# Kernel tuning notes

Hardware: AMD Instinct MI355X
Metric: run time of the kernel (lower is better)

The kernel has to match this reference:

```python
import jax, jax.numpy as jnp
import numpy as np

N_NODES = 50000
N_GRAPHS = 512


def gcn_conv(x, W, b, row, col, norm, n_nodes):
    # PyG GCNConv: h = x @ W; out_i = sum_{j->i} norm_ij * h_j + b
    h = x @ W  # [N, H]
    msgs = h[row] * norm[:, None]  # gather source features, scale
    out = jax.ops.segment_sum(msgs, col, num_segments=n_nodes)
    return out + b


def reference(x, edge_index, batch, W0, b0, W1, b1, W2, b2, Wf, bf):
    n = x.shape[0]
    src, dst = edge_index[0], edge_index[1]
    # add self loops
    loop = jnp.arange(n)
    row = jnp.concatenate([src, loop])
    col = jnp.concatenate([dst, loop])
    # symmetric degree normalization: 1/sqrt(deg_i * deg_j)
    deg = jax.ops.segment_sum(jnp.ones_like(col, dtype=x.dtype), col, num_segments=n)
    dis = jnp.where(deg > 0, 1.0 / jnp.sqrt(deg), 0.0)
    norm = dis[row] * dis[col]

    h = x
    for W, b in ((W0, b0), (W1, b1), (W2, b2)):
        h = jax.nn.relu(gcn_conv(h, W, b, row, col, norm, n))
        # dropout is identity in eval mode

    # global mean pool over graphs
    sums = jax.ops.segment_sum(h, batch, num_segments=N_GRAPHS)
    counts = jax.ops.segment_sum(jnp.ones((n,), dtype=h.dtype), batch, num_segments=N_GRAPHS)
    pooled = sums / jnp.maximum(counts, 1.0)[:, None]  # [B, H]

    logits = pooled @ Wf + bf
    return jax.nn.log_softmax(logits, axis=1)


def setup_inputs() -> dict:
    key = jax.random.key(0)
    ks = jax.random.split(key, 12)
    d_in, d_h, d_out = 128, 128, 10
    x = jax.random.normal(ks[0], (N_NODES, d_in), dtype=jnp.float32)
    edge_index = jax.random.randint(ks[1], (2, 600000), 0, N_NODES, dtype=jnp.int64)
    batch = jnp.sort(jax.random.randint(ks[2], (N_NODES,), 0, N_GRAPHS, dtype=jnp.int64))
    s = 1.0 / np.sqrt(d_h)
    return {
        "x": x,
        "edge_index": edge_index,
        "batch": batch,
        "W0": jax.random.normal(ks[3], (d_in, d_h), dtype=jnp.float32) * s,
        "b0": jnp.zeros((d_h,), dtype=jnp.float32),
        "W1": jax.random.normal(ks[4], (d_h, d_h), dtype=jnp.float32) * s,
        "b1": jnp.zeros((d_h,), dtype=jnp.float32),
        "W2": jax.random.normal(ks[5], (d_h, d_h), dtype=jnp.float32) * s,
        "b2": jnp.zeros((d_h,), dtype=jnp.float32),
        "Wf": jax.random.normal(ks[6], (d_h, d_out), dtype=jnp.float32) * s,
        "bf": jnp.zeros((d_out,), dtype=jnp.float32),
    }
```

## Files before the change

### kernel.cpp

```cpp
#include <hip/hip_runtime.h>
#include <hip/hip_bf16.h>

#define NN 50000
#define NE 600000
#define NG 512

typedef __attribute__((ext_vector_type(8))) short bf16x8;
typedef __attribute__((ext_vector_type(4))) float f32x4;

__device__ __forceinline__ float bf_lo(unsigned u) {
    unsigned v = u << 16;
    return __builtin_bit_cast(float, v);
}
__device__ __forceinline__ float bf_hi(unsigned u) {
    unsigned v = u & 0xFFFF0000u;
    return __builtin_bit_cast(float, v);
}
__device__ __forceinline__ unsigned f2bf(float f) {
    unsigned u = __builtin_bit_cast(unsigned, f);
    return (u + 0x7FFFu + ((u >> 16) & 1u)) >> 16;
}

__global__ __launch_bounds__(256) void k_zero(float* p, int n) {
    int i = blockIdx.x * 256 + threadIdx.x;
    if (i < n) p[i] = 0.0f;
}

__global__ __launch_bounds__(256) void k_histcnt(const int* __restrict__ dst, int* __restrict__ deg,
                                                 const int* __restrict__ batch, float* __restrict__ counts) {
    int i = blockIdx.x * 256 + threadIdx.x;
    if (i < NE) atomicAdd(&deg[dst[i]], 1);
    if (i < NN) atomicAdd(&counts[batch[i]], 1.0f);
}

__global__ __launch_bounds__(256) void k_alloc(const int* __restrict__ deg, int* __restrict__ gcur,
                                               int* __restrict__ rowstart, int* __restrict__ cursor,
                                               float* __restrict__ dis, uint2* __restrict__ cpk) {
    int i = blockIdx.x * 256 + threadIdx.x;
    if (i >= NN) return;
    int d = deg[i];
    int dr = (d + 7) & ~7;
    int st = atomicAdd(gcur, dr);
    rowstart[i] = st;
    cursor[i] = st;
    dis[i] = 1.0f / sqrtf((float)(d + 1));
    for (int p = st + d; p < st + dr; ++p) cpk[p] = make_uint2(0u, 0u);
}

__global__ __launch_bounds__(256) void k_fill(const int* __restrict__ src, const int* __restrict__ dst,
                                              const float* __restrict__ dis, int* __restrict__ cursor,
                                              uint2* __restrict__ cpk) {
    int e = blockIdx.x * 256 + threadIdx.x;
    if (e >= NE) return;
    int s = src[e], d = dst[e];
    int slot = atomicAdd(&cursor[d], 1);
    cpk[slot] = make_uint2((unsigned)s, __builtin_bit_cast(unsigned, dis[s] * dis[d]));
}

__global__ __launch_bounds__(256) void k_cvt_x(const float4* __restrict__ in, uint2* __restrict__ out, int n4) {
    int i = blockIdx.x * 256 + threadIdx.x;
    if (i >= n4) return;
    float4 v = in[i];
    uint2 o;
    o.x = f2bf(v.x) | (f2bf(v.y) << 16);
    o.y = f2bf(v.z) | (f2bf(v.w) << 16);
    out[i] = o;
}

__global__ __launch_bounds__(256) void k_cvt_w(const float* __restrict__ W0, const float* __restrict__ W1,
                                               const float* __restrict__ W2, unsigned short* __restrict__ Wt) {
    int idx = blockIdx.x * 256 + threadIdx.x;
    if (idx >= 3 * 16384) return;
    int m = idx >> 14;
    int r = idx & 16383;
    int k = r >> 7, c = r & 127;
    const float* W = (m == 0) ? W0 : (m == 1) ? W1 : W2;
    Wt[m * 16384 + c * 128 + k] = (unsigned short)f2bf(W[k * 128 + c]);
}

__global__ __launch_bounds__(256) void k_gemm_mfma(const unsigned short* __restrict__ A,
                                                   const unsigned short* __restrict__ Wt,
                                                   unsigned short* __restrict__ C, int M) {
    int wave = threadIdx.x >> 6;
    int lane = threadIdx.x & 63;
    int rowbase = blockIdx.x * 64 + wave * 16;
    int lr = lane & 15;
    int kg = lane >> 4;

    int arow = rowbase + lr;
    if (arow >= M) arow = M - 1;
    bf16x8 a[4];
#pragma unroll
    for (int kt = 0; kt < 4; ++kt)
        a[kt] = *(const bf16x8*)&A[arow * 128 + kt * 32 + kg * 8];

    f32x4 acc[8];
#pragma unroll
    for (int nt = 0; nt < 8; ++nt) acc[nt] = (f32x4){0.f, 0.f, 0.f, 0.f};

#pragma unroll
    for (int nt = 0; nt < 8; ++nt) {
        const unsigned short* wp = &Wt[(nt * 16 + lr) * 128 + kg * 8];
#pragma unroll
        for (int kt = 0; kt < 4; ++kt) {
            bf16x8 b = *(const bf16x8*)&wp[kt * 32];
            acc[nt] = __builtin_amdgcn_mfma_f32_16x16x32_bf16(a[kt], b, acc[nt], 0, 0, 0);
        }
    }

    int crow0 = rowbase + (lane >> 4) * 4;
#pragma unroll
    for (int nt = 0; nt < 8; ++nt) {
#pragma unroll
        for (int r = 0; r < 4; ++r) {
            int gr = crow0 + r;
            if (gr < M) C[gr * 128 + nt * 16 + lr] = (unsigned short)f2bf(acc[nt][r]);
        }
    }
}

template <int POOL>
__global__ __launch_bounds__(256) void k_gather(const uint2* __restrict__ h,
                                                const int* __restrict__ rowstart,
                                                const int* __restrict__ rowend,
                                                const uint2* __restrict__ cpk,
                                                const float* __restrict__ dis,
                                                const float* __restrict__ bias,
                                                uint2* __restrict__ outbuf,
                                                const int* __restrict__ batch,
                                                float* __restrict__ sums) {
    int t = blockIdx.x * 256 + threadIdx.x;
    int node = t >> 5;
    if (node >= NN) return;
    int f = t & 31;

    int s0 = rowstart[node];
    int e0 = rowend[node];

    float acc[8][4];
#pragma unroll
    for (int j = 0; j < 8; ++j)
#pragma unroll
        for (int k = 0; k < 4; ++k) acc[j][k] = 0.f;

    const uint4* mp = (const uint4*)cpk;
    uint4 m0, m1, m2, m3;
    {
        int b = s0 >> 1;
        m0 = mp[b]; m1 = mp[b + 1]; m2 = mp[b + 2]; m3 = mp[b + 3];
    }

    for (int s = s0; s < e0; s += 8) {
        uint4 c0 = m0, c1 = m1, c2 = m2, c3 = m3;
        int sn = s + 8;
        int b = (sn < e0 ? sn : s0) >> 1;
        m0 = mp[b]; m1 = mp[b + 1]; m2 = mp[b + 2]; m3 = mp[b + 3];

        uint2 v0 = h[(int)c0.x * 32 + f];
        uint2 v1 = h[(int)c0.z * 32 + f];
        uint2 v2 = h[(int)c1.x * 32 + f];
        uint2 v3 = h[(int)c1.z * 32 + f];
        uint2 v4 = h[(int)c2.x * 32 + f];
        uint2 v5 = h[(int)c2.z * 32 + f];
        uint2 v6 = h[(int)c3.x * 32 + f];
        uint2 v7 = h[(int)c3.z * 32 + f];
        float w0 = __builtin_bit_cast(float, c0.y);
        float w1 = __builtin_bit_cast(float, c0.w);
        float w2 = __builtin_bit_cast(float, c1.y);
        float w3 = __builtin_bit_cast(float, c1.w);
        float w4 = __builtin_bit_cast(float, c2.y);
        float w5 = __builtin_bit_cast(float, c2.w);
        float w6 = __builtin_bit_cast(float, c3.y);
        float w7 = __builtin_bit_cast(float, c3.w);

        acc[0][0] = fmaf(bf_lo(v0.x), w0, acc[0][0]);
        acc[0][1] = fmaf(bf_hi(v0.x), w0, acc[0][1]);
        acc[0][2] = fmaf(bf_lo(v0.y), w0, acc[0][2]);
        acc[0][3] = fmaf(bf_hi(v0.y), w0, acc[0][3]);
        acc[1][0] = fmaf(bf_lo(v1.x), w1, acc[1][0]);
        acc[1][1] = fmaf(bf_hi(v1.x), w1, acc[1][1]);
        acc[1][2] = fmaf(bf_lo(v1.y), w1, acc[1][2]);
        acc[1][3] = fmaf(bf_hi(v1.y), w1, acc[1][3]);
        acc[2][0] = fmaf(bf_lo(v2.x), w2, acc[2][0]);
        acc[2][1] = fmaf(bf_hi(v2.x), w2, acc[2][1]);
        acc[2][2] = fmaf(bf_lo(v2.y), w2, acc[2][2]);
        acc[2][3] = fmaf(bf_hi(v2.y), w2, acc[2][3]);
        acc[3][0] = fmaf(bf_lo(v3.x), w3, acc[3][0]);
        acc[3][1] = fmaf(bf_hi(v3.x), w3, acc[3][1]);
        acc[3][2] = fmaf(bf_lo(v3.y), w3, acc[3][2]);
        acc[3][3] = fmaf(bf_hi(v3.y), w3, acc[3][3]);
        acc[4][0] = fmaf(bf_lo(v4.x), w4, acc[4][0]);
        acc[4][1] = fmaf(bf_hi(v4.x), w4, acc[4][1]);
        acc[4][2] = fmaf(bf_lo(v4.y), w4, acc[4][2]);
        acc[4][3] = fmaf(bf_hi(v4.y), w4, acc[4][3]);
        acc[5][0] = fmaf(bf_lo(v5.x), w5, acc[5][0]);
        acc[5][1] = fmaf(bf_hi(v5.x), w5, acc[5][1]);
        acc[5][2] = fmaf(bf_lo(v5.y), w5, acc[5][2]);
        acc[5][3] = fmaf(bf_hi(v5.y), w5, acc[5][3]);
        acc[6][0] = fmaf(bf_lo(v6.x), w6, acc[6][0]);
        acc[6][1] = fmaf(bf_hi(v6.x), w6, acc[6][1]);
        acc[6][2] = fmaf(bf_lo(v6.y), w6, acc[6][2]);
        acc[6][3] = fmaf(bf_hi(v6.y), w6, acc[6][3]);
        acc[7][0] = fmaf(bf_lo(v7.x), w7, acc[7][0]);
        acc[7][1] = fmaf(bf_hi(v7.x), w7, acc[7][1]);
        acc[7][2] = fmaf(bf_lo(v7.y), w7, acc[7][2]);
        acc[7][3] = fmaf(bf_hi(v7.y), w7, acc[7][3]);
    }

    float d = dis[node];
    float ws = d * d;
    uint2 hv = h[node * 32 + f];
    acc[0][0] = fmaf(bf_lo(hv.x), ws, acc[0][0]);
    acc[0][1] = fmaf(bf_hi(hv.x), ws, acc[0][1]);
    acc[0][2] = fmaf(bf_lo(hv.y), ws, acc[0][2]);
    acc[0][3] = fmaf(bf_hi(hv.y), ws, acc[0][3]);

    float a0 = ((acc[0][0] + acc[1][0]) + (acc[2][0] + acc[3][0])) +
               ((acc[4][0] + acc[5][0]) + (acc[6][0] + acc[7][0]));
    float a1 = ((acc[0][1] + acc[1][1]) + (acc[2][1] + acc[3][1])) +
               ((acc[4][1] + acc[5][1]) + (acc[6][1] + acc[7][1]));
    float a2 = ((acc[0][2] + acc[1][2]) + (acc[2][2] + acc[3][2])) +
               ((acc[4][2] + acc[5][2]) + (acc[6][2] + acc[7][2]));
    float a3 = ((acc[0][3] + acc[1][3]) + (acc[2][3] + acc[3][3])) +
               ((acc[4][3] + acc[5][3]) + (acc[6][3] + acc[7][3]));

    float4 b = ((const float4*)bias)[f];
    a0 = fmaxf(a0 + b.x, 0.f);
    a1 = fmaxf(a1 + b.y, 0.f);
    a2 = fmaxf(a2 + b.z, 0.f);
    a3 = fmaxf(a3 + b.w, 0.f);

    if (POOL == 0) {
        uint2 o;
        o.x = f2bf(a0) | (f2bf(a1) << 16);
        o.y = f2bf(a2) | (f2bf(a3) << 16);
        outbuf[node * 32 + f] = o;
    } else {
        int g = batch[node];
        float* o = sums + g * 128 + f * 4;
        atomicAdd(o + 0, a0);
        atomicAdd(o + 1, a1);
        atomicAdd(o + 2, a2);
        atomicAdd(o + 3, a3);
    }
}

__global__ __launch_bounds__(64) void k_head(const float* __restrict__ sums,
                                             const float* __restrict__ counts,
                                             const float* __restrict__ Wf,
                                             const float* __restrict__ bf,
                                             float* __restrict__ out) {
    int g = blockIdx.x;
    int l = threadIdx.x;
    float inv = 1.0f / fmaxf(counts[g], 1.0f);
    float p0 = sums[g * 128 + l] * inv;
    float p1 = sums[g * 128 + 64 + l] * inv;
    float logit[10];
#pragma unroll
    for (int o = 0; o < 10; ++o) {
        float part = p0 * Wf[l * 10 + o] + p1 * Wf[(l + 64) * 10 + o];
#pragma unroll
        for (int s = 32; s > 0; s >>= 1) part += __shfl_xor(part, s);
        logit[o] = part + bf[o];
    }
    if (l == 0) {
        float m = logit[0];
#pragma unroll
        for (int o = 1; o < 10; ++o) m = fmaxf(m, logit[o]);
        float sum = 0.f;
#pragma unroll
        for (int o = 0; o < 10; ++o) sum += expf(logit[o] - m);
        float lse = m + logf(sum);
#pragma unroll
        for (int o = 0; o < 10; ++o) out[g * 10 + o] = logit[o] - lse;
    }
}

extern "C" void kernel_launch(void* const* d_in, const int* in_sizes, int n_in,
                              void* d_out, int out_size, void* d_ws, size_t ws_size,
                              hipStream_t stream) {
    const float* x     = (const float*)d_in[0];
    const int*   ei    = (const int*)d_in[1];
    const int*   batch = (const int*)d_in[2];
    const float* W0 = (const float*)d_in[3];
    const float* b0 = (const float*)d_in[4];
    const float* W1 = (const float*)d_in[5];
    const float* b1 = (const float*)d_in[6];
    const float* W2 = (const float*)d_in[7];
    const float* b2 = (const float*)d_in[8];
    const float* Wf = (const float*)d_in[9];
    const float* bf = (const float*)d_in[10];
    float* out = (float*)d_out;

    float* ws = (float*)d_ws;
    float* sums    = ws;
    float* counts  = ws + 65536;
    int*   in_deg  = (int*)(ws + 66048);
    int*   gcur    = (int*)(ws + 116096);
    float* dis     = ws + 116160;
    int*   rowstart= (int*)(ws + 166208);
    int*   cursor  = (int*)(ws + 216256);
    uint2* cpk     = (uint2*)(ws + 266304);
    unsigned short* Wt = (unsigned short*)(ws + 2166464);
    unsigned short* bx = (unsigned short*)(ws + 2191040);
    unsigned short* hA = (unsigned short*)(ws + 5391040);
    unsigned short* hB = (unsigned short*)(ws + 8591040);

    const int* src = ei;
    const int* dst = ei + NE;

    k_zero<<<(116160 + 255) / 256, 256, 0, stream>>>(ws, 116160);
    k_histcnt<<<2344, 256, 0, stream>>>(dst, in_deg, batch, counts);
    k_alloc<<<196, 256, 0, stream>>>(in_deg, gcur, rowstart, cursor, dis, cpk);
    k_fill<<<2344, 256, 0, stream>>>(src, dst, dis, cursor, cpk);
    k_cvt_x<<<6250, 256, 0, stream>>>((const float4*)x, (uint2*)bx, NN * 32);
    k_cvt_w<<<192, 256, 0, stream>>>(W0, W1, W2, Wt);

    const int GEMM_GRID = (NN + 63) / 64;

    k_gemm_mfma<<<GEMM_GRID, 256, 0, stream>>>(bx, Wt, hB, NN);
    k_gather<0><<<6250, 256, 0, stream>>>((const uint2*)hB, rowstart, cursor, cpk,
                                          dis, b0, (uint2*)hA, batch, sums);
    k_gemm_mfma<<<GEMM_GRID, 256, 0, stream>>>(hA, Wt + 16384, hB, NN);
    k_gather<0><<<6250, 256, 0, stream>>>((const uint2*)hB, rowstart, cursor, cpk,
                                          dis, b1, (uint2*)hA, batch, sums);
    k_gemm_mfma<<<GEMM_GRID, 256, 0, stream>>>(hA, Wt + 32768, hB, NN);
    k_gather<1><<<6250, 256, 0, stream>>>((const uint2*)hB, rowstart, cursor, cpk,
                                          dis, b2, nullptr, batch, sums);

    k_head<<<512, 64, 0, stream>>>(sums, counts, Wf, bf, out);
}
```

Before: 373.1 us.

## Replace gather aggregation with push-to-edge-message buffer plus contiguous segmented sum

Builds a source-indexed CSR that maps each edge to its destination slot. Per layer, each source node scales its features by the edge weight and writes one bf16 message per edge into a destination-ordered buffer, and a second kernel sums contiguous messages per node. Random reads become random writes followed by sequential reads. The cost is a 600k×128 bf16 message buffer written and read every layer, extra atomics and CSR setup, and message values rounded to bf16 before summation. The new path runs only when the workspace is large enough; otherwise the old gather path is kept.

After: 517.3 us. +38.6%, slower.

```diff
diff --git a/kernel.cpp b/kernel.cpp
--- a/kernel.cpp
+++ b/kernel.cpp
@@ -26,35 +26,49 @@
     if (i < n) p[i] = 0.0f;
 }
 
-__global__ __launch_bounds__(256) void k_histcnt(const int* __restrict__ dst, int* __restrict__ deg,
+__global__ __launch_bounds__(256) void k_histcnt(const int* __restrict__ src, const int* __restrict__ dst,
+                                                 int* __restrict__ in_deg, int* __restrict__ out_deg,
                                                  const int* __restrict__ batch, float* __restrict__ counts) {
     int i = blockIdx.x * 256 + threadIdx.x;
-    if (i < NE) atomicAdd(&deg[dst[i]], 1);
+    if (i < NE) {
+        atomicAdd(&in_deg[dst[i]], 1);
+        atomicAdd(&out_deg[src[i]], 1);
+    }
     if (i < NN) atomicAdd(&counts[batch[i]], 1.0f);
 }
 
-__global__ __launch_bounds__(256) void k_alloc(const int* __restrict__ deg, int* __restrict__ gcur,
+__global__ __launch_bounds__(256) void k_alloc(const int* __restrict__ in_deg, const int* __restrict__ out_deg,
+                                               int* __restrict__ gcur,
                                                int* __restrict__ rowstart, int* __restrict__ cursor,
-                                               float* __restrict__ dis, uint2* __restrict__ cpk) {
+                                               int* __restrict__ srowstart, int* __restrict__ scursor,
+                                               float* __restrict__ dis, uint2* __restrict__ cpk, int pad) {
     int i = blockIdx.x * 256 + threadIdx.x;
     if (i >= NN) return;
-    int d = deg[i];
-    int dr = (d + 7) & ~7;
+    int d = in_deg[i];
+    int dr = (d + pad - 1) & ~(pad - 1);
     int st = atomicAdd(gcur, dr);
     rowstart[i] = st;
     cursor[i] = st;
     dis[i] = 1.0f / sqrtf((float)(d + 1));
     for (int p = st + d; p < st + dr; ++p) cpk[p] = make_uint2(0u, 0u);
+    int od = out_deg[i];
+    int sst = atomicAdd(gcur + 1, od);
+    srowstart[i] = sst;
+    scursor[i] = sst;
 }
 
 __global__ __launch_bounds__(256) void k_fill(const int* __restrict__ src, const int* __restrict__ dst,
                                               const float* __restrict__ dis, int* __restrict__ cursor,
-                                              uint2* __restrict__ cpk) {
+                                              int* __restrict__ scursor,
+                                              uint2* __restrict__ cpk, uint2* __restrict__ scsr) {
     int e = blockIdx.x * 256 + threadIdx.x;
     if (e >= NE) return;
     int s = src[e], d = dst[e];
+    float w = dis[s] * dis[d];
     int slot = atomicAdd(&cursor[d], 1);
-    cpk[slot] = make_uint2((unsigned)s, __builtin_bit_cast(unsigned, dis[s] * dis[d]));
+    cpk[slot] = make_uint2((unsigned)s, __builtin_bit_cast(unsigned, w));
+    int sslot = atomicAdd(&scursor[s], 1);
+    scsr[sslot] = make_uint2((unsigned)slot, __builtin_bit_cast(unsigned, w));
 }
 
 __global__ __launch_bounds__(256) void k_cvt_x(const float4* __restrict__ in, uint2* __restrict__ out, int n4) {
@@ -116,6 +130,93 @@
             int gr = crow0 + r;
             if (gr < M) C[gr * 128 + nt * 16 + lr] = (unsigned short)f2bf(acc[nt][r]);
         }
+    }
+}
+
+__global__ __launch_bounds__(256) void k_push(const uint2* __restrict__ h,
+                                              const int* __restrict__ srowstart,
+                                              const int* __restrict__ srowend,
+                                              const uint2* __restrict__ scsr,
+                                              uint2* __restrict__ msg) {
+    int t = blockIdx.x * 256 + threadIdx.x;
+    int node = t >> 5;
+    if (node >= NN) return;
+    int f = t & 31;
+    uint2 hv = h[node * 32 + f];
+    float h0 = bf_lo(hv.x), h1 = bf_hi(hv.x), h2 = bf_lo(hv.y), h3 = bf_hi(hv.y);
+    int s = srowstart[node];
+    int e = srowend[node];
+    for (; s < e; ++s) {
+        uint2 q = scsr[s];
+        float w = __builtin_bit_cast(float, q.y);
+        uint2 o;
+        o.x = f2bf(h0 * w) | (f2bf(h1 * w) << 16);
+        o.y = f2bf(h2 * w) | (f2bf(h3 * w) << 16);
+        msg[(int)q.x * 32 + f] = o;
+    }
+}
+
+template <int POOL>
+__global__ __launch_bounds__(256) void k_sum(const uint2* __restrict__ msg,
+                                             const uint2* __restrict__ h,
+                                             const int* __restrict__ rowstart,
+                                             const int* __restrict__ rowend,
+                                             const float* __restrict__ dis,
+                                             const float* __restrict__ bias,
+                                             uint2* __restrict__ outbuf,
+                                             const int* __restrict__ batch,
+                                             float* __restrict__ sums) {
+    int t = blockIdx.x * 256 + threadIdx.x;
+    int node = t >> 5;
+    if (node >= NN) return;
+    int f = t & 31;
+
+    float d = dis[node];
+    float ws = d * d;
+    uint2 hv = h[node * 32 + f];
+    float a0 = bf_lo(hv.x) * ws;
+    float a1 = bf_hi(hv.x) * ws;
+    float a2 = bf_lo(hv.y) * ws;
+    float a3 = bf_hi(hv.y) * ws;
+
+    int s = rowstart[node];
+    int e = rowend[node];
+    for (; s + 3 < e; s += 4) {
+        uint2 m0 = msg[(s + 0) * 32 + f];
+        uint2 m1 = msg[(s + 1) * 32 + f];
+        uint2 m2 = msg[(s + 2) * 32 + f];
+        uint2 m3 = msg[(s + 3) * 32 + f];
+        a0 += bf_lo(m0.x) + bf_lo(m1.x) + bf_lo(m2.x) + bf_lo(m3.x);
+        a1 += bf_hi(m0.x) + bf_hi(m1.x) + bf_hi(m2.x) + bf_hi(m3.x);
+        a2 += bf_lo(m0.y) + bf_lo(m1.y) + bf_lo(m2.y) + bf_lo(m3.y);
+        a3 += bf_hi(m0.y) + bf_hi(m1.y) + bf_hi(m2.y) + bf_hi(m3.y);
+    }
+    for (; s < e; ++s) {
+        uint2 m = msg[s * 32 + f];
+        a0 += bf_lo(m.x);
+        a1 += bf_hi(m.x);
+        a2 += bf_lo(m.y);
+        a3 += bf_hi(m.y);
+    }
+
+    float4 b = ((const float4*)bias)[f];
+    a0 = fmaxf(a0 + b.x, 0.f);
+    a1 = fmaxf(a1 + b.y, 0.f);
+    a2 = fmaxf(a2 + b.z, 0.f);
+    a3 = fmaxf(a3 + b.w, 0.f);
+
+    if (POOL == 0) {
+        uint2 o;
+        o.x = f2bf(a0) | (f2bf(a1) << 16);
+        o.y = f2bf(a2) | (f2bf(a3) << 16);
+        outbuf[node * 32 + f] = o;
+    } else {
+        int g = batch[node];
+        float* o = sums + g * 128 + f * 4;
+        atomicAdd(o + 0, a0);
+        atomicAdd(o + 1, a1);
+        atomicAdd(o + 2, a2);
+        atomicAdd(o + 3, a3);
     }
 }
 
@@ -293,40 +394,64 @@
     float* out = (float*)d_out;
 
     float* ws = (float*)d_ws;
-    float* sums    = ws;
-    float* counts  = ws + 65536;
-    int*   in_deg  = (int*)(ws + 66048);
-    int*   gcur    = (int*)(ws + 116096);
-    float* dis     = ws + 116160;
-    int*   rowstart= (int*)(ws + 166208);
-    int*   cursor  = (int*)(ws + 216256);
-    uint2* cpk     = (uint2*)(ws + 266304);
-    unsigned short* Wt = (unsigned short*)(ws + 2166464);
-    unsigned short* bx = (unsigned short*)(ws + 2191040);
-    unsigned short* hA = (unsigned short*)(ws + 5391040);
-    unsigned short* hB = (unsigned short*)(ws + 8591040);
+    float* sums     = ws;
+    float* counts   = ws + 65536;
+    int*   in_deg   = (int*)(ws + 66048);
+    int*   out_deg  = (int*)(ws + 116096);
+    int*   gcur     = (int*)(ws + 166144);
+    float* dis      = ws + 166208;
+    int*   rowstart = (int*)(ws + 216256);
+    int*   cursor   = (int*)(ws + 266304);
+    int*   srowstart= (int*)(ws + 316352);
+    int*   scursor  = (int*)(ws + 366400);
+    uint2* cpk      = (uint2*)(ws + 416448);
+    uint2* scsr     = (uint2*)(ws + 2316608);
+    unsigned short* Wt = (unsigned short*)(ws + 3516736);
+    unsigned short* bx = (unsigned short*)(ws + 3541312);
+    unsigned short* hA = (unsigned short*)(ws + 6741312);
+    unsigned short* hB = (unsigned short*)(ws + 9941312);
+    uint2* msg      = (uint2*)(ws + 13141312);
+
+    const bool use_msg = ws_size >= (size_t)51545408 * 4;
+    const int pad = use_msg ? 1 : 8;
 
     const int* src = ei;
     const int* dst = ei + NE;
 
-    k_zero<<<(116160 + 255) / 256, 256, 0, stream>>>(ws, 116160);
-    k_histcnt<<<2344, 256, 0, stream>>>(dst, in_deg, batch, counts);
-    k_alloc<<<196, 256, 0, stream>>>(in_deg, gcur, rowstart, cursor, dis, cpk);
-    k_fill<<<2344, 256, 0, stream>>>(src, dst, dis, cursor, cpk);
+    k_zero<<<(166208 + 255) / 256, 256, 0, stream>>>(ws, 166208);
+    k_histcnt<<<2344, 256, 0, stream>>>(src, dst, in_deg, out_deg, batch, counts);
+    k_alloc<<<196, 256, 0, stream>>>(in_deg, out_deg, gcur, rowstart, cursor,
+                                     srowstart, scursor, dis, cpk, pad);
+    k_fill<<<2344, 256, 0, stream>>>(src, dst, dis, cursor, scursor, cpk, scsr);
     k_cvt_x<<<6250, 256, 0, stream>>>((const float4*)x, (uint2*)bx, NN * 32);
     k_cvt_w<<<192, 256, 0, stream>>>(W0, W1, W2, Wt);
 
     const int GEMM_GRID = (NN + 63) / 64;
 
-    k_gemm_mfma<<<GEMM_GRID, 256, 0, stream>>>(bx, Wt, hB, NN);
-    k_gather<0><<<6250, 256, 0, stream>>>((const uint2*)hB, rowstart, cursor, cpk,
-                                          dis, b0, (uint2*)hA, batch, sums);
-    k_gemm_mfma<<<GEMM_GRID, 256, 0, stream>>>(hA, Wt + 16384, hB, NN);
-    k_gather<0><<<6250, 256, 0, stream>>>((const uint2*)hB, rowstart, cursor, cpk,
-                                          dis, b1, (uint2*)hA, batch, sums);
-    k_gemm_mfma<<<GEMM_GRID, 256, 0, stream>>>(hA, Wt + 32768, hB, NN);
-    k_gather<1><<<6250, 256, 0, stream>>>((const uint2*)hB, rowstart, cursor, cpk,
-                                          dis, b2, nullptr, batch, sums);
+    if (use_msg) {
+        k_gemm_mfma<<<GEMM_GRID, 256, 0, stream>>>(bx, Wt, hB, NN);
+        k_push<<<6250, 256, 0, stream>>>((const uint2*)hB, srowstart, scursor, scsr, msg);
+        k_sum<0><<<6250, 256, 0, stream>>>(msg, (const uint2*)hB, rowstart, cursor,
+                                           dis, b0, (uint2*)hA, batch, sums);
+        k_gemm_mfma<<<GEMM_GRID, 256, 0, stream>>>(hA, Wt + 16384, hB, NN);
+        k_push<<<6250, 256, 0, stream>>>((const uint2*)hB, srowstart, scursor, scsr, msg);
+        k_sum<0><<<6250, 256, 0, stream>>>(msg, (const uint2*)hB, rowstart, cursor,
+                                           dis, b1, (uint2*)hA, batch, sums);
+        k_gemm_mfma<<<GEMM_GRID, 256, 0, stream>>>(hA, Wt + 32768, hB, NN);
+        k_push<<<6250, 256, 0, stream>>>((const uint2*)hB, srowstart, scursor, scsr, msg);
+        k_sum<1><<<6250, 256, 0, stream>>>(msg, (const uint2*)hB, rowstart, cursor,
+                                           dis, b2, nullptr, batch, sums);
+    } else {
+        k_gemm_mfma<<<GEMM_GRID, 256, 0, stream>>>(bx, Wt, hB, NN);
+        k_gather<0><<<6250, 256, 0, stream>>>((const uint2*)hB, rowstart, cursor, cpk,
+                                              dis, b0, (uint2*)hA, batch, sums);
+        k_gemm_mfma<<<GEMM_GRID, 256, 0, stream>>>(hA, Wt + 16384, hB, NN);
+        k_gather<0><<<6250, 256, 0, stream>>>((const uint2*)hB, rowstart, cursor, cpk,
+                                              dis, b1, (uint2*)hA, batch, sums);
+        k_gemm_mfma<<<GEMM_GRID, 256, 0, stream>>>(hA, Wt + 32768, hB, NN);
+        k_gather<1><<<6250, 256, 0, stream>>>((const uint2*)hB, rowstart, cursor, cpk,
+                                              dis, b2, nullptr, batch, sums);
+    }
 
     k_head<<<512, 64, 0, stream>>>(sums, counts, Wf, bf, out);
 }
```
